# Performance work log

Measured on AMD Instinct MI355X. Metric: run time of the kernel, lower is better.

Reference implementation:

```python
import jax, jax.numpy as jnp
import numpy as np


def setup_inputs() -> dict:
    key = jax.random.key(0)
    k1, k2, k3, k4 = jax.random.split(key, 4)
    N, D, C = 131072, 128, 1024
    inputs = jax.random.normal(k1, (N, D), dtype=jnp.float32)
    centers = jax.random.normal(k2, (C, D), dtype=jnp.float32)
    gamma = jax.random.uniform(k3, (1,), dtype=jnp.float32)
    normalization = jax.random.normal(k4, (C, C), dtype=jnp.float32)
    return {"inputs": inputs, "centers": centers, "gamma": gamma,
            "normalization": normalization}


def _gaussian_kernel(inputs, centers, gamma):
    # Flatten trailing dims: [N, D]
    x = inputs.reshape(inputs.shape[0], -1)
    x2 = jnp.sum(x * x, axis=-1, keepdims=True)            # [N, 1]
    c2 = jnp.sum(centers * centers, axis=-1)               # [C]
    cross = x @ centers.T                                  # [N, C]
    sqd = jnp.maximum(x2 + c2[None, :] - 2.0 * cross, 0.0)  # [N, C]
    return jnp.exp(-gamma * sqd)


def reference(inputs, centers, gamma, normalization):
    densities = _gaussian_kernel(inputs, centers, gamma[0])  # [N, C]
    return densities @ normalization                          # [N, C]
```

## Files before the change

kernel.cpp:

```cpp
#include <hip/hip_runtime.h>
#include <hip/hip_fp8.h>
#include <stdint.h>

typedef float    f32x4  __attribute__((ext_vector_type(4)));
typedef float    f32x16 __attribute__((ext_vector_type(16)));
typedef int      i32x4  __attribute__((ext_vector_type(4)));
typedef int      i32x8  __attribute__((ext_vector_type(8)));
typedef __bf16   bf16x8 __attribute__((ext_vector_type(8)));
typedef uint16_t u16x8  __attribute__((ext_vector_type(8)));
typedef uint16_t u16x4  __attribute__((ext_vector_type(4)));
typedef uint8_t  u8x4   __attribute__((ext_vector_type(4)));
typedef uint32_t u32x4  __attribute__((ext_vector_type(4)));

static __device__ __forceinline__ f32x4 mfma_bf16(bf16x8 a, bf16x8 b, f32x4 c) {
  return __builtin_amdgcn_mfma_f32_16x16x32_bf16(a, b, c, 0, 0, 0);
}
static __device__ __forceinline__ uint16_t f2bf(float f) {
  uint32_t u = __builtin_bit_cast(uint32_t, f);
  u += 0x7fffu + ((u >> 16) & 1u);
  return (uint16_t)(u >> 16);
}
static __device__ __forceinline__ uint8_t f2fp8(float f) {
  __hip_fp8_e4m3 v(f);
  return v.__x;
}
static __device__ __forceinline__ void gload16(const void* src, void* lds) {
  __builtin_amdgcn_global_load_lds(
      (const __attribute__((address_space(1))) void*)src,
      (__attribute__((address_space(3))) void*)lds, 16, 0, 0);
}

constexpr int Nrows = 131072;
constexpr int Dk    = 128;
constexpr int Cc    = 1024;
constexpr int CH     = 16384;
constexpr int NCHUNK = Nrows / CH;
constexpr int BMf   = 64;
constexpr int BNf   = 256;
constexpr int KBf   = 128;
constexpr int XBYTES = BMf * Dk * 2;
constexpr int PBYTES = BMf * KBf * 2;
constexpr int LDS_MAIN = XBYTES + PBYTES + BMf * 4;
constexpr int LDS_FB   = LDS_MAIN + Cc * 4;
constexpr int KEXP2_LDS = 32768 * 3 + 128 * 144 + 512;

__global__ void prep_cen(const float* __restrict__ cen,
                         uint16_t* __restrict__ cenb,
                         float* __restrict__ c2) {
  const int t = threadIdx.x;
  const int row = blockIdx.x * 16 + (t >> 4);
  const int q = t & 15;
  const float* src = cen + (size_t)row * Dk + q * 8;
  f32x4 v0 = *(const f32x4*)src;
  f32x4 v1 = *(const f32x4*)(src + 4);
  u16x8 h;
  float ss = 0.f;
#pragma unroll
  for (int i = 0; i < 4; ++i) {
    h[i]     = f2bf(v0[i]); ss += v0[i] * v0[i];
    h[i + 4] = f2bf(v1[i]); ss += v1[i] * v1[i];
  }
  *(u16x8*)(cenb + (size_t)row * Dk + q * 8) = h;
  ss += __shfl_xor(ss, 1);
  ss += __shfl_xor(ss, 2);
  ss += __shfl_xor(ss, 4);
  ss += __shfl_xor(ss, 8);
  if (q == 0) c2[row] = ss;
}

__global__ void prep_nT8(const float* __restrict__ nrm, uint8_t* __restrict__ nT8) {
  __shared__ float tile[64][65];
  const int jb = blockIdx.x & 15;
  const int cb = blockIdx.x >> 4;
  const int t  = threadIdx.x;
  const int r  = t >> 4;
  const int q  = t & 15;
#pragma unroll
  for (int i = 0; i < 4; ++i) {
    int row = r + i * 16;
    f32x4 v = *(const f32x4*)(nrm + (size_t)(cb * 64 + row) * Cc + jb * 64 + q * 4);
#pragma unroll
    for (int s = 0; s < 4; ++s) tile[row][q * 4 + s] = v[s];
  }
  __syncthreads();
#pragma unroll
  for (int i = 0; i < 4; ++i) {
    int j = r + i * 16;
    u8x4 hs;
#pragma unroll
    for (int s = 0; s < 4; ++s) hs[s] = f2fp8(tile[q * 4 + s][j]);
    *(u8x4*)(nT8 + (size_t)(jb * 64 + j) * Cc + cb * 64 + q * 4) = hs;
  }
}

__global__ void prep_nT(const float* __restrict__ nrm, uint16_t* __restrict__ nT) {
  __shared__ float tile[64][65];
  const int jb = blockIdx.x & 15;
  const int cb = blockIdx.x >> 4;
  const int t  = threadIdx.x;
  const int r  = t >> 4;
  const int q  = t & 15;
#pragma unroll
  for (int i = 0; i < 4; ++i) {
    int row = r + i * 16;
    f32x4 v = *(const f32x4*)(nrm + (size_t)(cb * 64 + row) * Cc + jb * 64 + q * 4);
#pragma unroll
    for (int s = 0; s < 4; ++s) tile[row][q * 4 + s] = v[s];
  }
  __syncthreads();
#pragma unroll
  for (int i = 0; i < 4; ++i) {
    int j = r + i * 16;
    u16x4 hs;
#pragma unroll
    for (int s = 0; s < 4; ++s) hs[s] = f2bf(tile[q * 4 + s][j]);
    *(u16x4*)(nT + (size_t)(jb * 64 + j) * Cc + cb * 64 + q * 4) = hs;
  }
}

__global__ __launch_bounds__(512, 2) void kexp2(
    const float* __restrict__ x, const float* __restrict__ gam,
    const uint16_t* __restrict__ cenb, const float* __restrict__ c2g,
    uint8_t* __restrict__ P, int row0) {
  extern __shared__ char smem[];
  char*    xB   = smem;
  char*    cB0  = smem + 32768;
  char*    cB1  = smem + 65536;
  uint8_t* pbuf = (uint8_t*)(smem + 98304);
  float*   x2s  = (float*)(smem + 98304 + 128 * 144);

  const int tid  = threadIdx.x;
  const int lane = tid & 63;
  const int wid  = tid >> 6;
  const int wr   = wid >> 2;
  const int wn   = wid & 3;
  const int l15  = lane & 15;
  const int l4   = lane >> 4;
  const int mb   = blockIdx.x;

  auto stage_c = [&](char* db, int ct) {
#pragma unroll
    for (int i = 0; i < 4; ++i) {
      int ch = tid + i * 512;
      int r  = ch >> 4;
      int c  = ch & 15;
      gload16(cenb + (size_t)(ct * 128 + r) * Dk + ((c ^ (r & 7)) * 8),
              db + ch * 16);
    }
  };
  stage_c(cB0, 0);

  const float* xblk = x + (size_t)(row0 + mb * 128) * Dk;
#pragma unroll
  for (int it = 0; it < 4; ++it) {
    int ch = tid + it * 512;
    int r  = ch >> 4;
    int cc = ch & 15;
    const float* src = xblk + r * Dk + cc * 8;
    f32x4 v0 = __builtin_nontemporal_load((const f32x4*)src);
    f32x4 v1 = __builtin_nontemporal_load((const f32x4*)(src + 4));
    u16x8 hh;
    float ss = 0.f;
#pragma unroll
    for (int i = 0; i < 4; ++i) {
      hh[i]     = f2bf(v0[i]); ss += v0[i] * v0[i];
      hh[i + 4] = f2bf(v1[i]); ss += v1[i] * v1[i];
    }
    *(u16x8*)(xB + r * 256 + ((cc ^ (r & 7)) * 16)) = hh;
    ss += __shfl_xor(ss, 1);
    ss += __shfl_xor(ss, 2);
    ss += __shfl_xor(ss, 4);
    ss += __shfl_xor(ss, 8);
    if ((tid & 15) == 0) x2s[r] = ss;
  }

  const float ngam = -gam[0];

  for (int ct = 0; ct < 8; ++ct) {
    char* cC = (ct & 1) ? cB1 : cB0;
    char* cN = (ct & 1) ? cB0 : cB1;
    if (ct < 7) stage_c(cN, ct + 1);
    if (ct == 0 || ct == 7) asm volatile("s_waitcnt vmcnt(4)" ::: "memory");
    else                    asm volatile("s_waitcnt vmcnt(8)" ::: "memory");
    __builtin_amdgcn_s_barrier();

    f32x4 cr[4][2];
#pragma unroll
    for (int m = 0; m < 4; ++m)
#pragma unroll
      for (int n = 0; n < 2; ++n) cr[m][n] = f32x4{0.f, 0.f, 0.f, 0.f};

#pragma unroll
    for (int kk = 0; kk < 4; ++kk) {
      bf16x8 aF[4], bF[2];
#pragma unroll
      for (int m = 0; m < 4; ++m) {
        int row = wr * 64 + m * 16 + l15;
        aF[m] = *(const bf16x8*)(xB + row * 256 +
                                 (((kk * 4 + l4) ^ (row & 7)) * 16));
      }
#pragma unroll
      for (int n = 0; n < 2; ++n) {
        int col = wn * 32 + n * 16 + l15;
        bF[n] = *(const bf16x8*)(cC + col * 256 +
                                 (((kk * 4 + l4) ^ (col & 7)) * 16));
      }
#pragma unroll
      for (int m = 0; m < 4; ++m)
#pragma unroll
        for (int n = 0; n < 2; ++n) cr[m][n] = mfma_bf16(aF[m], bF[n], cr[m][n]);
    }

    float c2v[2];
#pragma unroll
    for (int n = 0; n < 2; ++n) c2v[n] = c2g[ct * 128 + wn * 32 + n * 16 + l15];
#pragma unroll
    for (int m = 0; m < 4; ++m) {
#pragma unroll
      for (int n = 0; n < 2; ++n) {
#pragma unroll
        for (int rr = 0; rr < 4; ++rr) {
          int row = wr * 64 + m * 16 + l4 * 4 + rr;
          float s = fmaxf(fmaf(-2.f, cr[m][n][rr], x2s[row] + c2v[n]), 0.f);
          pbuf[row * 144 + wn * 32 + n * 16 + l15] = f2fp8(__expf(ngam * s));
        }
      }
    }
    __builtin_amdgcn_s_barrier();
#pragma unroll
    for (int it = 0; it < 2; ++it) {
      int ch = tid + it * 512;
      int r  = ch >> 3;
      int c  = ch & 7;
      *(u32x4*)(P + (size_t)(mb * 128 + r) * Cc + ct * 128 + c * 16) =
          *(const u32x4*)(pbuf + r * 144 + c * 16);
    }
  }
}

__global__ __launch_bounds__(512, 2) void g2f8(
    const uint8_t* __restrict__ P, const uint8_t* __restrict__ nT8,
    float* __restrict__ out, int row0, int mblocks) {
  extern __shared__ char smem[];
  char* a0 = smem;
  char* b0 = smem + 16384;
  char* a1 = smem + 32768;
  char* b1 = smem + 49152;

  const int tid  = threadIdx.x;
  const int lane = tid & 63;
  const int wid  = tid >> 6;
  const int wm   = wid >> 2;
  const int wn   = wid & 3;
  const int l31  = lane & 31;
  const int lh   = lane >> 5;

  const int nwg  = mblocks * 4;
  const int cpx  = nwg >> 3;
  const int wgid = (blockIdx.x & 7) * cpx + (blockIdx.x >> 3);
  const int nb   = wgid & 3;
  const int mb   = wgid >> 2;

  const uint8_t* Abase = P + (size_t)mb * 256 * Cc;
  const uint8_t* Bbase = nT8 + (size_t)nb * 256 * Cc;

  auto stage = [&](const uint8_t* gb, char* db, int k0) {
#pragma unroll
    for (int i = 0; i < 2; ++i) {
      int ch = tid + i * 512;
      int r  = ch >> 2;
      int c  = ch & 3;
      gload16(gb + (size_t)r * Cc + k0 + c * 16, db + ch * 16);
    }
  };

  f32x16 acc[4][2];
#pragma unroll
  for (int m = 0; m < 4; ++m)
#pragma unroll
    for (int n = 0; n < 2; ++n)
#pragma unroll
      for (int r = 0; r < 16; ++r) acc[m][n][r] = 0.f;

  stage(Bbase, b0, 0);
  stage(Abase, a0, 0);
  stage(Bbase, b1, 64);

  auto ldfrag = [&](const char* base, int off) -> i32x8 {
    i32x4 lo = *(const i32x4*)(base + off);
    i32x4 hi = *(const i32x4*)(base + off + 16);
    return __builtin_shufflevector(lo, hi, 0, 1, 2, 3, 4, 5, 6, 7);
  };

  for (int kt = 0; kt < 16; ++kt) {
    const int q = kt & 1;
    char* aC = q ? a1 : a0;
    char* bC = q ? b1 : b0;
    char* aN = q ? a0 : a1;

    if (kt == 15) asm volatile("s_waitcnt vmcnt(0)" ::: "memory");
    else          asm volatile("s_waitcnt vmcnt(2)" ::: "memory");
    __builtin_amdgcn_s_barrier();

    if (kt + 1 < 16) stage(Abase, aN, (kt + 1) * 64);

    i32x8 bF[2];
#pragma unroll
    for (int n = 0; n < 2; ++n)
      bF[n] = ldfrag(bC, (wn * 64 + n * 32 + l31) * 64 + lh * 32);

    {
      i32x8 aF = ldfrag(aC, (wm * 128 + l31) * 64 + lh * 32);
      __builtin_amdgcn_s_setprio(1);
      acc[0][0] = __builtin_amdgcn_mfma_scale_f32_32x32x64_f8f6f4(
          aF, bF[0], acc[0][0], 0, 0, 0, 127, 0, 127);
      acc[0][1] = __builtin_amdgcn_mfma_scale_f32_32x32x64_f8f6f4(
          aF, bF[1], acc[0][1], 0, 0, 0, 127, 0, 127);
      __builtin_amdgcn_s_setprio(0);
    }
    __builtin_amdgcn_s_barrier();
    if (kt + 2 < 16) stage(Bbase, bC, (kt + 2) * 64);

    __builtin_amdgcn_s_setprio(1);
#pragma unroll
    for (int m = 1; m < 4; ++m) {
      i32x8 aF = ldfrag(aC, (wm * 128 + m * 32 + l31) * 64 + lh * 32);
      acc[m][0] = __builtin_amdgcn_mfma_scale_f32_32x32x64_f8f6f4(
          aF, bF[0], acc[m][0], 0, 0, 0, 127, 0, 127);
      acc[m][1] = __builtin_amdgcn_mfma_scale_f32_32x32x64_f8f6f4(
          aF, bF[1], acc[m][1], 0, 0, 0, 127, 0, 127);
    }
    __builtin_amdgcn_s_setprio(0);
  }

  float* obuf = (float*)smem;
#pragma unroll
  for (int h = 0; h < 4; ++h) {
    __syncthreads();
    if (wm == (h >> 1)) {
      const int mbase = (h & 1) * 2;
#pragma unroll
      for (int ml = 0; ml < 2; ++ml) {
#pragma unroll
        for (int n = 0; n < 2; ++n) {
#pragma unroll
          for (int r = 0; r < 16; ++r) {
            int rin = (r & 3) + 8 * (r >> 2) + 4 * lh;
            obuf[(ml * 32 + rin) * 256 + wn * 64 + n * 32 + l31] =
                acc[mbase + ml][n][r];
          }
        }
      }
    }
    __syncthreads();
#pragma unroll
    for (int i = 0; i < 8; ++i) {
      int ch = tid + i * 512;
      int rL = ch >> 6;
      int c4 = ch & 63;
      *(f32x4*)(out + (size_t)(row0 + mb * 256 + h * 64 + rL) * Cc +
                nb * 256 + c4 * 4) = *(const f32x4*)(obuf + rL * 256 + c4 * 4);
    }
  }
}

template <int USE_NT>
__global__ __launch_bounds__(512, 4) void nyst_main(
    const float* __restrict__ x, const float* __restrict__ cen,
    const float* __restrict__ gam, const float* __restrict__ nrm,
    const uint16_t* __restrict__ cenb, const float* __restrict__ c2g,
    const uint16_t* __restrict__ nT, float* __restrict__ out) {
  extern __shared__ char smem[];
  char*  xB  = smem;
  char*  pB  = smem + XBYTES;
  float* x2s = (float*)(smem + XBYTES + PBYTES);
  float* c2s = (float*)(smem + LDS_MAIN);

  const int tid  = threadIdx.x;
  const int lane = tid & 63;
  const int wid  = tid >> 6;
  const int wr   = wid >> 2;
  const int wc   = wid & 3;
  const int xcd  = blockIdx.x & 7;
  const int bi   = blockIdx.x >> 3;
  const int colb = xcd >> 1;
  const int rowb = (bi << 1) | (xcd & 1);
  const int l15  = lane & 15;
  const int l4   = lane >> 4;

  const float* xblk = x + (size_t)rowb * BMf * Dk;

#pragma unroll
  for (int it = 0; it < 2; ++it) {
    int ch = tid + it * 512;
    int r  = ch >> 4;
    int cc = ch & 15;
    const float* src = xblk + r * Dk + cc * 8;
    f32x4 v0 = __builtin_nontemporal_load((const f32x4*)src);
    f32x4 v1 = __builtin_nontemporal_load((const f32x4*)(src + 4));
    u16x8 hh;
    float ss = 0.f;
#pragma unroll
    for (int i = 0; i < 4; ++i) {
      hh[i]     = f2bf(v0[i]); ss += v0[i] * v0[i];
      hh[i + 4] = f2bf(v1[i]); ss += v1[i] * v1[i];
    }
    int off = (r * 256 + cc * 16) ^ ((r & 7) << 4);
    *(u16x8*)(xB + off) = hh;
    ss += __shfl_xor(ss, 1);
    ss += __shfl_xor(ss, 2);
    ss += __shfl_xor(ss, 4);
    ss += __shfl_xor(ss, 8);
    if ((tid & 15) == 0) x2s[r] = ss;
  }
  if (!USE_NT) {
#pragma unroll
    for (int rr = 0; rr < 2; ++rr) {
      int r = tid + rr * 512;
      const float* src = cen + (size_t)r * Dk;
      float ss = 0.f;
      for (int k = 0; k < Dk / 4; ++k) {
        f32x4 v = *(const f32x4*)(src + 4 * k);
        ss += v[0] * v[0] + v[1] * v[1] + v[2] * v[2] + v[3] * v[3];
      }
      c2s[r] = ss;
    }
  }
  __syncthreads();

  const float ngam = -gam[0];
  f32x4 zero4 = {0.f, 0.f, 0.f, 0.f};
  f32x4 acc[2][4];
#pragma unroll
  for (int m = 0; m < 2; ++m)
#pragma unroll
    for (int n = 0; n < 4; ++n) acc[m][n] = zero4;

  for (int c0 = 0; c0 < Cc; c0 += KBf) {
    f32x4 cr[2][2];
#pragma unroll
    for (int g = 0; g < 2; ++g)
#pragma unroll
      for (int m = 0; m < 2; ++m) cr[g][m] = zero4;

#pragma unroll
    for (int kk = 0; kk < 4; ++kk) {
      bf16x8 b0, b1;
      if (USE_NT) {
        int c0col = c0 + 16 * wc + l15;
        b0 = *(const bf16x8*)(cenb + (size_t)c0col * Dk + kk * 32 + l4 * 8);
        b1 = *(const bf16x8*)(cenb + (size_t)(c0col + 64) * Dk + kk * 32 + l4 * 8);
      } else {
#pragma unroll
        for (int g = 0; g < 2; ++g) {
          int ccol = c0 + g * 64 + 16 * wc + l15;
          const float* cb_ = cen + (size_t)ccol * Dk + kk * 32 + l4 * 8;
          f32x4 v0 = *(const f32x4*)cb_;
          f32x4 v1 = *(const f32x4*)(cb_ + 4);
          u16x8 tt;
#pragma unroll
          for (int i = 0; i < 4; ++i) { tt[i] = f2bf(v0[i]); tt[i + 4] = f2bf(v1[i]); }
          if (g == 0) b0 = __builtin_bit_cast(bf16x8, tt);
          else        b1 = __builtin_bit_cast(bf16x8, tt);
        }
      }
#pragma unroll
      for (int m = 0; m < 2; ++m) {
        int row = 32 * wr + 16 * m + l15;
        int off = (row * 256 + kk * 64 + l4 * 16) ^ ((row & 7) << 4);
        bf16x8 a = *(const bf16x8*)(xB + off);
        cr[0][m] = mfma_bf16(a, b0, cr[0][m]);
        cr[1][m] = mfma_bf16(a, b1, cr[1][m]);
      }
    }

    __syncthreads();
#pragma unroll
    for (int g = 0; g < 2; ++g) {
      int ccol = c0 + g * 64 + 16 * wc + l15;
      float c2v = USE_NT ? c2g[ccol] : c2s[ccol];
#pragma unroll
      for (int m = 0; m < 2; ++m) {
#pragma unroll
        for (int r = 0; r < 4; ++r) {
          int row = 32 * wr + 16 * m + l4 * 4 + r;
          float s = fmaxf(fmaf(-2.f, cr[g][m][r], x2s[row] + c2v), 0.f);
          float p = __expf(ngam * s);
          int off = (row * 256 + (g * 64 + 16 * wc + l15) * 2) ^ ((row & 7) << 4);
          *(uint16_t*)(pB + off) = f2bf(p);
        }
      }
    }
    __syncthreads();

#pragma unroll
    for (int kk = 0; kk < 4; ++kk) {
      bf16x8 pa[2];
#pragma unroll
      for (int m = 0; m < 2; ++m) {
        int row = 32 * wr + 16 * m + l15;
        int off = (row * 256 + kk * 64 + l4 * 16) ^ ((row & 7) << 4);
        pa[m] = *(const bf16x8*)(pB + off);
      }
      int krow = c0 + kk * 32 + l4 * 8;
#pragma unroll
      for (int n = 0; n < 4; ++n) {
        int j = colb * BNf + wc * 64 + 16 * n + l15;
        bf16x8 bm;
        if (USE_NT) {
          bm = *(const bf16x8*)(nT + (size_t)j * Cc + krow);
        } else {
          u16x8 tt;
#pragma unroll
          for (int i = 0; i < 8; ++i) tt[i] = f2bf(nrm[(size_t)(krow + i) * Cc + j]);
          bm = __builtin_bit_cast(bf16x8, tt);
        }
        acc[0][n] = mfma_bf16(pa[0], bm, acc[0][n]);
        acc[1][n] = mfma_bf16(pa[1], bm, acc[1][n]);
      }
    }
  }

  float* outBuf = (float*)smem;
  const int orow0 = rowb * BMf;
#pragma unroll
  for (int h = 0; h < 2; ++h) {
    __syncthreads();
    if (wr == h) {
#pragma unroll
      for (int m = 0; m < 2; ++m) {
#pragma unroll
        for (int n = 0; n < 4; ++n) {
#pragma unroll
          for (int r = 0; r < 4; ++r) {
            int rL = 16 * m + l4 * 4 + r;
            outBuf[rL * 256 + wc * 64 + 16 * n + l15] = acc[m][n][r];
          }
        }
      }
    }
    __syncthreads();
#pragma unroll
    for (int i = 0; i < 4; ++i) {
      int ch = tid + 512 * i;
      int rL = ch >> 6;
      int c4 = ch & 63;
      f32x4 v = *(const f32x4*)(outBuf + rL * 256 + c4 * 4);
      *(f32x4*)(out + (size_t)(orow0 + 32 * h + rL) * Cc + colb * BNf + c4 * 4) = v;
    }
  }
}

extern "C" void kernel_launch(void* const* d_in, const int* in_sizes, int n_in,
                              void* d_out, int out_size, void* d_ws, size_t ws_size,
                              hipStream_t stream) {
  const float* x   = (const float*)d_in[0];
  const float* cen = (const float*)d_in[1];
  const float* gam = (const float*)d_in[2];
  const float* nrm = (const float*)d_in[3];
  float* out = (float*)d_out;

  const size_t cenbB = (size_t)Cc * Dk * 2;
  const size_t c2B   = (size_t)Cc * 4;
  const size_t nT8B  = (size_t)Cc * Cc;
  const size_t nTB   = (size_t)Cc * Cc * 2;
  const size_t pFull = (size_t)Nrows * Cc;
  const size_t pChB  = (size_t)CH * Cc;

  if (ws_size >= cenbB + c2B + nT8B + pFull) {
    uint16_t* cenb = (uint16_t*)d_ws;
    float*    c2   = (float*)((char*)d_ws + cenbB);
    uint8_t*  nT8  = (uint8_t*)((char*)d_ws + cenbB + c2B);
    uint8_t*  Pws  = (uint8_t*)((char*)d_ws + cenbB + c2B + nT8B);
    prep_cen<<<64, 256, 0, stream>>>(cen, cenb, c2);
    prep_nT8<<<256, 256, 0, stream>>>(nrm, nT8);
    kexp2<<<Nrows / 128, 512, KEXP2_LDS, stream>>>(x, gam, cenb, c2, Pws, 0);
    g2f8<<<(Nrows / 256) * 4, 512, 65536, stream>>>(Pws, nT8, out, 0, Nrows / 256);
  } else if (ws_size >= cenbB + c2B + nT8B + pChB) {
    uint16_t* cenb = (uint16_t*)d_ws;
    float*    c2   = (float*)((char*)d_ws + cenbB);
    uint8_t*  nT8  = (uint8_t*)((char*)d_ws + cenbB + c2B);
    uint8_t*  Pws  = (uint8_t*)((char*)d_ws + cenbB + c2B + nT8B);
    prep_cen<<<64, 256, 0, stream>>>(cen, cenb, c2);
    prep_nT8<<<256, 256, 0, stream>>>(nrm, nT8);
    for (int c = 0; c < NCHUNK; ++c) {
      kexp2<<<CH / 128, 512, KEXP2_LDS, stream>>>(x, gam, cenb, c2, Pws, c * CH);
      g2f8<<<(CH / 256) * 4, 512, 65536, stream>>>(Pws, nT8, out, c * CH, CH / 256);
    }
  } else if (ws_size >= cenbB + c2B + nTB) {
    uint16_t* cenb = (uint16_t*)d_ws;
    float*    c2   = (float*)((char*)d_ws + cenbB);
    uint16_t* nT   = (uint16_t*)((char*)d_ws + cenbB + c2B);
    prep_cen<<<64, 256, 0, stream>>>(cen, cenb, c2);
    prep_nT<<<256, 256, 0, stream>>>(nrm, nT);
    nyst_main<1><<<(Nrows / BMf) * (Cc / BNf), 512, LDS_MAIN, stream>>>(
        x, cen, gam, nrm, cenb, c2, nT, out);
  } else {
    nyst_main<0><<<(Nrows / BMf) * (Cc / BNf), 512, LDS_FB, stream>>>(
        x, cen, gam, nrm, nullptr, nullptr, nullptr, out);
  }
}
```

Measured before the change: 329.8 us.

## Load B fragments directly from global into registers in fp8 GEMM

The second GEMM kernel stops staging the B (normalization) tile through LDS and instead has each wave load its B fragments straight from global memory into double-buffered registers. Only A is staged in LDS, which halves shared-memory use per block and removes the second mid-iteration B staging step. The wait is now a full vmcnt(0) each iteration, which reduces how much load latency overlaps with compute. B reads also become uncoalesced per-lane 32-byte loads, with the same data fetched redundantly by the waves that share a column block.

```diff
diff --git a/kernel.cpp b/kernel.cpp
--- a/kernel.cpp
+++ b/kernel.cpp
@@ -243,9 +243,7 @@
     float* __restrict__ out, int row0, int mblocks) {
   extern __shared__ char smem[];
   char* a0 = smem;
-  char* b0 = smem + 16384;
-  char* a1 = smem + 32768;
-  char* b1 = smem + 49152;
+  char* a1 = smem + 16384;
 
   const int tid  = threadIdx.x;
   const int lane = tid & 63;
@@ -262,75 +260,67 @@
   const int mb   = wgid >> 2;
 
   const uint8_t* Abase = P + (size_t)mb * 256 * Cc;
-  const uint8_t* Bbase = nT8 + (size_t)nb * 256 * Cc;
-
-  auto stage = [&](const uint8_t* gb, char* db, int k0) {
+  const uint8_t* Bp = nT8 + (size_t)(nb * 256 + wn * 64 + l31) * Cc + lh * 32;
+
+  auto stageA = [&](char* db, int k0) {
 #pragma unroll
     for (int i = 0; i < 2; ++i) {
       int ch = tid + i * 512;
       int r  = ch >> 2;
       int c  = ch & 3;
-      gload16(gb + (size_t)r * Cc + k0 + c * 16, db + ch * 16);
+      gload16(Abase + (size_t)r * Cc + k0 + c * 16, db + ch * 16);
     }
   };
-
-  f32x16 acc[4][2];
-#pragma unroll
-  for (int m = 0; m < 4; ++m)
-#pragma unroll
-    for (int n = 0; n < 2; ++n)
-#pragma unroll
-      for (int r = 0; r < 16; ++r) acc[m][n][r] = 0.f;
-
-  stage(Bbase, b0, 0);
-  stage(Abase, a0, 0);
-  stage(Bbase, b1, 64);
-
-  auto ldfrag = [&](const char* base, int off) -> i32x8 {
+  auto loadB = [&](i32x8 (&bf)[2], int k0) {
+#pragma unroll
+    for (int n = 0; n < 2; ++n) {
+      const uint8_t* p = Bp + (size_t)(n * 32) * Cc + k0;
+      i32x4 lo = *(const i32x4*)p;
+      i32x4 hi = *(const i32x4*)(p + 16);
+      bf[n] = __builtin_shufflevector(lo, hi, 0, 1, 2, 3, 4, 5, 6, 7);
+    }
+  };
+  auto ldfragA = [&](const char* base, int off) -> i32x8 {
     i32x4 lo = *(const i32x4*)(base + off);
     i32x4 hi = *(const i32x4*)(base + off + 16);
     return __builtin_shufflevector(lo, hi, 0, 1, 2, 3, 4, 5, 6, 7);
   };
 
-  for (int kt = 0; kt < 16; ++kt) {
-    const int q = kt & 1;
-    char* aC = q ? a1 : a0;
-    char* bC = q ? b1 : b0;
-    char* aN = q ? a0 : a1;
-
-    if (kt == 15) asm volatile("s_waitcnt vmcnt(0)" ::: "memory");
-    else          asm volatile("s_waitcnt vmcnt(2)" ::: "memory");
+  f32x16 acc[4][2];
+#pragma unroll
+  for (int m = 0; m < 4; ++m)
+#pragma unroll
+    for (int n = 0; n < 2; ++n)
+#pragma unroll
+      for (int r = 0; r < 16; ++r) acc[m][n][r] = 0.f;
+
+  i32x8 bfA[2], bfB[2];
+  loadB(bfA, 0);
+  stageA(a0, 0);
+
+  auto tile = [&](char* aC, char* aN, i32x8 (&bU)[2], i32x8 (&bL)[2], int kt) {
+    asm volatile("s_waitcnt vmcnt(0)" ::: "memory");
     __builtin_amdgcn_s_barrier();
-
-    if (kt + 1 < 16) stage(Abase, aN, (kt + 1) * 64);
-
-    i32x8 bF[2];
-#pragma unroll
-    for (int n = 0; n < 2; ++n)
-      bF[n] = ldfrag(bC, (wn * 64 + n * 32 + l31) * 64 + lh * 32);
-
-    {
-      i32x8 aF = ldfrag(aC, (wm * 128 + l31) * 64 + lh * 32);
-      __builtin_amdgcn_s_setprio(1);
-      acc[0][0] = __builtin_amdgcn_mfma_scale_f32_32x32x64_f8f6f4(
-          aF, bF[0], acc[0][0], 0, 0, 0, 127, 0, 127);
-      acc[0][1] = __builtin_amdgcn_mfma_scale_f32_32x32x64_f8f6f4(
-          aF, bF[1], acc[0][1], 0, 0, 0, 127, 0, 127);
-      __builtin_amdgcn_s_setprio(0);
-    }
+    if (kt + 1 < 16) {
+      loadB(bL, (kt + 1) * 64);
+      stageA(aN, (kt + 1) * 64);
+    }
+    __builtin_amdgcn_s_setprio(1);
+#pragma unroll
+    for (int m = 0; m < 4; ++m) {
+      i32x8 aF = ldfragA(aC, (wm * 128 + m * 32 + l31) * 64 + lh * 32);
+      acc[m][0] = __builtin_amdgcn_mfma_scale_f32_32x32x64_f8f6f4(
+          aF, bU[0], acc[m][0], 0, 0, 0, 127, 0, 127);
+      acc[m][1] = __builtin_amdgcn_mfma_scale_f32_32x32x64_f8f6f4(
+          aF, bU[1], acc[m][1], 0, 0, 0, 127, 0, 127);
+    }
+    __builtin_amdgcn_s_setprio(0);
     __builtin_amdgcn_s_barrier();
-    if (kt + 2 < 16) stage(Bbase, bC, (kt + 2) * 64);
-
-    __builtin_amdgcn_s_setprio(1);
-#pragma unroll
-    for (int m = 1; m < 4; ++m) {
-      i32x8 aF = ldfrag(aC, (wm * 128 + m * 32 + l31) * 64 + lh * 32);
-      acc[m][0] = __builtin_amdgcn_mfma_scale_f32_32x32x64_f8f6f4(
-          aF, bF[0], acc[m][0], 0, 0, 0, 127, 0, 127);
-      acc[m][1] = __builtin_amdgcn_mfma_scale_f32_32x32x64_f8f6f4(
-          aF, bF[1], acc[m][1], 0, 0, 0, 127, 0, 127);
-    }
-    __builtin_amdgcn_s_setprio(0);
+  };
+
+  for (int kt2 = 0; kt2 < 8; ++kt2) {
+    tile(a0, a1, bfA, bfB, 2 * kt2);
+    tile(a1, a0, bfB, bfA, 2 * kt2 + 1);
   }
 
   float* obuf = (float*)smem;
```

New measurement: 408.1 us. 1.24x slower.
